# Optimization experiments

Hardware: AMD Instinct MI355X
Metric: run time of the kernel (lower is better)

## Reference

```python
import jax, jax.numpy as jnp
import numpy as np

B, S = 128, 64          # batch, sequence length (cities)
H = 128                 # hidden size
STATIC, DYNAMIC = 2, 2  # static/dynamic feature channels


def setup_inputs() -> dict:
    key = jax.random.key(0)
    ks = jax.random.split(key, 16)
    g = lambda k, shape: (jax.random.normal(k, shape, dtype=jnp.float32) * 0.1)
    return {
        "static": jax.random.normal(ks[0], (B, STATIC, S), dtype=jnp.float32),
        "dynamic": jax.random.uniform(ks[1], (B, DYNAMIC, S), dtype=jnp.float32),
        "x0": jnp.zeros((STATIC,), jnp.float32),           # learned initial decoder input
        "static_w": g(ks[2], (H, STATIC)),  "static_b": g(ks[3], (H,)),
        "dynamic_w": g(ks[4], (H, DYNAMIC)), "dynamic_b": g(ks[5], (H,)),
        "decoder_w": g(ks[6], (H, STATIC)), "decoder_b": g(ks[7], (H,)),
        "gru_wih": g(ks[8], (3 * H, H)), "gru_whh": g(ks[9], (3 * H, H)),
        "gru_bih": g(ks[10], (3 * H,)), "gru_bhh": g(ks[11], (3 * H,)),
        "attn_v": g(ks[12], (H,)), "attn_W": g(ks[13], (H, 3 * H)),
        "ptr_v": g(ks[14], (H,)),  "ptr_W": g(ks[15], (H, 2 * H)),
    }


def _forward(static, dynamic, x0, static_w, static_b, dynamic_w, dynamic_b,
             decoder_w, decoder_b, gru_wih, gru_whh, gru_bih, gru_bhh,
             attn_v, attn_W, ptr_v, ptr_W):
    Bsz, in_size, seq = static.shape
    # Conv1d with kernel_size=1 == pointwise channel mixing
    conv = lambda w, b, x: jnp.einsum('oi,bis->bos', w, x) + b[None, :, None]
    static_h = conv(static_w, static_b, static)      # [B,H,S]
    dynamic_h = conv(dynamic_w, dynamic_b, dynamic)  # [B,H,S]

    def gru_cell(x, h):
        # torch nn.GRU gate order: r, z, n
        gi = x @ gru_wih.T + gru_bih
        gh = h @ gru_whh.T + gru_bhh
        i_r, i_z, i_n = jnp.split(gi, 3, axis=1)
        h_r, h_z, h_n = jnp.split(gh, 3, axis=1)
        r = jax.nn.sigmoid(i_r + h_r)
        z = jax.nn.sigmoid(i_z + h_z)
        n = jnp.tanh(i_n + r * h_n)
        return (1.0 - z) * n + z * h

    def step(carry, _):
        dec_in, h = carry                                   # [B,in,1], [B,H]
        dec_h = conv(decoder_w, decoder_b, dec_in)[:, :, 0]  # [B,H]
        h_new = gru_cell(dec_h, h)                           # rnn_out == last_hh (1 layer)
        rnn_out = h_new
        # encoder attention over cities
        hid = jnp.concatenate(
            [static_h, dynamic_h,
             jnp.broadcast_to(rnn_out[:, :, None], static_h.shape)], axis=1)  # [B,3H,S]
        e = jnp.tanh(jnp.einsum('hk,bks->bhs', attn_W, hid))
        attns = jax.nn.softmax(jnp.einsum('h,bhs->bs', attn_v, e), axis=1)    # [B,S]
        context = jnp.einsum('bs,bhs->bh', attns, static_h)                   # [B,H]
        energy = jnp.concatenate(
            [static_h, jnp.broadcast_to(context[:, :, None], static_h.shape)], axis=1)
        logits = jnp.einsum('h,bhs->bs', ptr_v,
                            jnp.tanh(jnp.einsum('hk,bks->bhs', ptr_W, energy)))
        # mask_fn is None -> mask stays all ones -> mask.log() == 0
        logp_all = jax.nn.log_softmax(logits, axis=1)
        ptr = jnp.argmax(logp_all, axis=1)                  # greedy (eval mode)
        logp = jnp.take_along_axis(logp_all, ptr[:, None], axis=1)[:, 0]
        idx = jnp.broadcast_to(ptr[:, None, None], (Bsz, in_size, 1))
        new_in = jax.lax.stop_gradient(jnp.take_along_axis(static, idx, axis=2))
        return (new_in, h_new), (ptr, logp)

    dec0 = jnp.broadcast_to(x0[None, :, None], (Bsz, in_size, 1))
    h0 = jnp.zeros((Bsz, static_h.shape[1]), static.dtype)
    _, (ptrs, logps) = jax.lax.scan(step, (dec0, h0), None, length=seq)
    return ptrs.T, logps.T  # tour_idx [B,S] int, tour_logp [B,S] float


def reference(static, dynamic, x0, static_w, static_b, dynamic_w, dynamic_b,
              decoder_w, decoder_b, gru_wih, gru_whh, gru_bih, gru_bhh,
              attn_v, attn_W, ptr_v, ptr_W):
    return _forward(static, dynamic, x0, static_w, static_b, dynamic_w, dynamic_b,
                    decoder_w, decoder_b, gru_wih, gru_whh, gru_bih, gru_bhh,
                    attn_v, attn_W, ptr_v, ptr_W)
```

## Files before the change

### kernel.cpp

```cpp
#include <hip/hip_runtime.h>
#include <math.h>


#define K1  1.44269504088896340736f
#define K2  2.88539008177792681472f
#define LN2 0.69314718055994530942f

#define WS_M     0
#define WS_C     768
#define WS_PREA  1152
#define WS_PREP  (WS_PREA + 128*8192)
#define WS_Q     (WS_PREP + 128*8192)

template <int CTRL>
__device__ __forceinline__ float dppk(float x) {
  int xi = __builtin_bit_cast(int, x);
  return __builtin_bit_cast(float,
      __builtin_amdgcn_update_dpp(xi, xi, CTRL, 0xF, 0xF, false));
}
template <int CTRL>
__device__ __forceinline__ float dppz(float x) {
  int xi = __builtin_bit_cast(int, x);
  return __builtin_bit_cast(float,
      __builtin_amdgcn_update_dpp(0, xi, CTRL, 0xF, 0xF, true));
}
__device__ __forceinline__ float bcastf(float x, int lane) {
  return __builtin_bit_cast(float,
      __builtin_amdgcn_readlane(__builtin_bit_cast(int, x), lane));
}
__device__ __forceinline__ float sum4(float x) {
  x += dppk<0xB1>(x); x += dppk<0x4E>(x); return x;
}
__device__ __forceinline__ float sum8(float x) {
  x += dppk<0xB1>(x); x += dppk<0x4E>(x); x += dppk<0x141>(x); return x;
}
__device__ __forceinline__ float wsum64(float x) {
  x += dppz<0x111>(x); x += dppz<0x112>(x); x += dppz<0x114>(x);
  x += dppz<0x118>(x); x += dppz<0x142>(x); x += dppz<0x143>(x);
  return bcastf(x, 63);
}
__device__ __forceinline__ float wmax64(float x) {
  x = fmaxf(x, dppk<0x111>(x)); x = fmaxf(x, dppk<0x112>(x));
  x = fmaxf(x, dppk<0x114>(x)); x = fmaxf(x, dppk<0x118>(x));
  x = fmaxf(x, dppk<0x142>(x)); x = fmaxf(x, dppk<0x143>(x));
  return bcastf(x, 63);
}
#define RCP(x)  __builtin_amdgcn_rcpf(x)
#define EXP2(x) __builtin_amdgcn_exp2f(x)

__device__ __forceinline__ void bar_lds() {
  asm volatile("s_waitcnt lgkmcnt(0)" ::: "memory");
  __builtin_amdgcn_s_barrier();
  asm volatile("" ::: "memory");
}

__device__ __forceinline__ int rot8(int p) {
  return (p & 56) | ((p + (p >> 3)) & 7);
}

__global__ __launch_bounds__(256) void prep_small(
    const float* __restrict__ wih, const float* __restrict__ decw,
    const float* __restrict__ decb, const float* __restrict__ bih,
    float* __restrict__ ws) {
  int gid = blockIdx.x * 256 + threadIdx.x;
  if (gid < 384) {
    float m0 = 0.f, m1 = 0.f, cc = 0.f;
    for (int k = 0; k < 128; ++k) {
      float w = wih[gid * 128 + k];
      m0 += w * decw[k * 2 + 0];
      m1 += w * decw[k * 2 + 1];
      cc += w * decb[k];
    }
    ws[WS_M + gid * 2 + 0] = m0;
    ws[WS_M + gid * 2 + 1] = m1;
    ws[WS_C + gid] = cc + bih[gid];
  }
}

__global__ __launch_bounds__(256) void prep_big(
    const float* __restrict__ statics, const float* __restrict__ dynamics,
    const float* __restrict__ sw, const float* __restrict__ sb,
    const float* __restrict__ dw, const float* __restrict__ db,
    const float* __restrict__ attn_W, const float* __restrict__ ptr_W,
    float* __restrict__ ws) {
  __shared__ __align__(16) float sh[128 * 64];
  __shared__ __align__(16) float dh[128 * 64];
  __shared__ float st[128];
  __shared__ float dy[128];
  int b = blockIdx.x >> 3;
  int hq = blockIdx.x & 7;
  int t = threadIdx.x;
  if (t < 128) st[t] = statics[b * 128 + t];
  else         dy[t - 128] = dynamics[b * 128 + (t - 128)];
  __syncthreads();
  for (int e = t; e < 8192; e += 256) {
    int h = e >> 6, s = e & 63;
    sh[e] = sw[h * 2 + 0] * st[s] + sw[h * 2 + 1] * st[64 + s] + sb[h];
    dh[e] = dw[h * 2 + 0] * dy[s] + dw[h * 2 + 1] * dy[64 + s] + db[h];
  }
  __syncthreads();
  int hh = hq * 16 + (t >> 4);
  int s0 = (t & 15) * 4;
  float4 pA = {0, 0, 0, 0}, pP = {0, 0, 0, 0}, qq = {0, 0, 0, 0};
  for (int k = 0; k < 128; ++k) {
    float4 sv = *(const float4*)&sh[k * 64 + s0];
    float4 dv = *(const float4*)&dh[k * 64 + s0];
    float w1 = attn_W[hh * 384 + k];
    float w2 = attn_W[hh * 384 + 128 + k];
    float p1 = ptr_W[hh * 256 + k];
    float p2 = ptr_W[hh * 256 + 128 + k];
    pA.x += w1 * sv.x + w2 * dv.x;  pA.y += w1 * sv.y + w2 * dv.y;
    pA.z += w1 * sv.z + w2 * dv.z;  pA.w += w1 * sv.w + w2 * dv.w;
    pP.x += p1 * sv.x;  pP.y += p1 * sv.y;  pP.z += p1 * sv.z;  pP.w += p1 * sv.w;
    qq.x += p2 * sv.x;  qq.y += p2 * sv.y;  qq.z += p2 * sv.z;  qq.w += p2 * sv.w;
  }
  float4 eA, eP;
  eA.x = exp2f(K2 * pA.x); eA.y = exp2f(K2 * pA.y);
  eA.z = exp2f(K2 * pA.z); eA.w = exp2f(K2 * pA.w);
  eP.x = exp2f(K2 * pP.x); eP.y = exp2f(K2 * pP.y);
  eP.z = exp2f(K2 * pP.z); eP.w = exp2f(K2 * pP.w);
  int o = b * 8192 + hh * 64 + s0;
  *(float4*)&ws[WS_PREA + o] = eA;
  *(float4*)&ws[WS_PREP + o] = eP;
  *(float4*)&ws[WS_Q + o]    = qq;
}

__global__ __launch_bounds__(512)
__attribute__((amdgpu_waves_per_eu(2)))
void drl4tsp_main(
    const float* __restrict__ statics, const float* __restrict__ x0,
    const float* __restrict__ whh, const float* __restrict__ attn_W,
    const float* __restrict__ bhh_g, const float* __restrict__ attn_v,
    const float* __restrict__ ptr_v, const float* __restrict__ ws,
    float* __restrict__ out) {
  __shared__ float4 W3s4[128 * 32];
  __shared__ float4 EAT4[64 * 32];
  __shared__ float4 EPT4[64 * 32];
  __shared__ float4 uav3[64];
  __shared__ float4 uav2[64];
  __shared__ float4 gp4[128 * 3];
  __shared__ __align__(16) float hp[144];
  __shared__ __align__(16) float attns[64];
  __shared__ float a_lds[64];
  __shared__ float l_lds[64];
  __shared__ float stt[128];
  __shared__ float outbuf[64];
  __shared__ float Lhist[4096];

  const int b    = blockIdx.x;
  const int t    = threadIdx.x;
  const int lane = t & 63;
  const int g    = t >> 2;
  const int q    = t & 3;
  const int s    = t >> 3;
  const int hg   = t & 7;

  float wr0[32], wr1[32], wr2[32];
#pragma unroll
  for (int kk = 0; kk < 8; ++kk) {
    float4 a = *(const float4*)(whh + g * 128         + kk * 16 + q * 4);
    float4 c = *(const float4*)(whh + (128 + g) * 128 + kk * 16 + q * 4);
    float4 d = *(const float4*)(whh + (256 + g) * 128 + kk * 16 + q * 4);
    wr0[4*kk] = a.x; wr0[4*kk+1] = a.y; wr0[4*kk+2] = a.z; wr0[4*kk+3] = a.w;
    wr1[4*kk] = c.x; wr1[4*kk+1] = c.y; wr1[4*kk+2] = c.z; wr1[4*kk+3] = c.w;
    wr2[4*kk] = d.x; wr2[4*kk+1] = d.y; wr2[4*kk+2] = d.z; wr2[4*kk+3] = d.w;
  }
  float qr[16];
  {
    const float4* pq = (const float4*)(ws + WS_Q + b * 8192 + g * 64 + q * 16);
#pragma unroll
    for (int i = 0; i < 4; ++i) {
      float4 v = pq[i];
      qr[4*i] = v.x; qr[4*i+1] = v.y; qr[4*i+2] = v.z; qr[4*i+3] = v.w;
    }
  }

  {
    const float4* src = (const float4*)(attn_W + g * 384 + 256);
#pragma unroll
    for (int kk = 0; kk < 8; ++kk) {
      int j = q * 8 + kk;
      W3s4[g * 32 + ((j + 2 * g) & 31)] = src[j];
    }
  }
  for (int e = t; e < 8192; e += 512) {
    int h = e >> 6, sE = e & 63;
    int rg = ((h >> 2) + sE) & 31;
    ((float*)EAT4)[sE * 128 + rg * 4 + (h & 3)] = ws[WS_PREA + b * 8192 + e];
    ((float*)EPT4)[sE * 128 + rg * 4 + (h & 3)] = ws[WS_PREP + b * 8192 + e];
  }
  if (t < 128) {
    int h = t;
    int rg = rot8(h >> 1);
    ((float*)uav3)[rg * 4 + (h & 1) * 2 + 1] = 2.0f * attn_v[h];
    ((float*)uav2)[rg * 4 + (h & 1) * 2 + 1] = 2.0f * ptr_v[h];
    stt[h] = statics[b * 128 + h];
    const float* Mm = ws + WS_M;
    const float* Cc = ws + WS_C;
    float cR = Cc[h] + bhh_g[h];
    float cZ = Cc[128 + h] + bhh_g[128 + h];
    gp4[h*3 + 0] = float4{Mm[h*2], Mm[h*2+1], cR, Mm[(128+h)*2]};
    gp4[h*3 + 1] = float4{Mm[(128+h)*2+1], cZ, Mm[(256+h)*2], Mm[(256+h)*2+1]};
    gp4[h*3 + 2] = float4{Cc[256+h], bhh_g[256+h], 0.f, 0.f};
  }
  __syncthreads();

  float hreg = 0.f, ghr = 0.f, ghz = 0.f, ghn = 0.f;
  float d0 = x0[0], d1 = x0[1];

  for (int step = 0; step < 64; ++step) {
    {
      float4 v0 = gp4[g*3], v1 = gp4[g*3+1], v2 = gp4[g*3+2];
      float r = RCP(1.f + EXP2(-K1 * (v0.x*d0 + v0.y*d1 + v0.z + ghr)));
      float z = RCP(1.f + EXP2(-K1 * (v0.w*d0 + v1.x*d1 + v1.y + ghz)));
      float xn = v1.z*d0 + v1.w*d1 + v2.x + r * (ghn + v2.y);
      float n = 1.f - 2.f * RCP(EXP2(K2 * xn) + 1.f);
      hreg = (1.f - z) * n + z * hreg;
      if (q == 0) hp[(g >> 5) * 36 + (g & 31)] = hreg;
    }
    bar_lds();
    {
      float u3a = 0.f, u3b = 0.f;
#pragma unroll
      for (int kk = 0; kk < 8; ++kk) {
        float4 hv = *(const float4*)&hp[(kk >> 1) * 36 + (kk & 1) * 16 + q * 4];
        float4 wv = W3s4[g * 32 + ((kk * 4 + q + 2 * g) & 31)];
        float d2 = wv.x*hv.x + wv.y*hv.y + wv.z*hv.z + wv.w*hv.w;
        if (kk & 1) u3b += d2; else u3a += d2;
      }
      float u3 = sum4(u3a + u3b);
      if (q == 0)
        ((float*)uav3)[rot8(g >> 1) * 4 + (g & 1) * 2] = EXP2(K2 * u3);
    }
    bar_lds();
    float sr = 0.f, sz = 0.f, sn = 0.f;
    {
      float acc0 = 0.f, acc1 = 0.f;
#pragma unroll
      for (int ii = 0; ii < 4; ++ii) {
        float4 ea = EAT4[s * 32 + ((hg * 4 + ii + s) & 31)];
        int p0 = hg * 8 + 2 * ii;
        float4 ua = uav3[(p0 & 56) | ((p0 + hg) & 7)];
        float4 ub = uav3[((p0+1) & 56) | ((p0 + 1 + hg) & 7)];
        float x1 = ea.x * ua.x + 1.f, y1 = ea.y * ua.z + 1.f;
        acc0 += (ua.y * y1 + ua.w * x1) * RCP(x1 * y1);
        float x2 = ea.z * ub.x + 1.f, y2 = ea.w * ub.z + 1.f;
        acc1 += (ub.y * y2 + ub.w * x2) * RCP(x2 * y2);
      }
#pragma unroll
      for (int kk = 0; kk < 4; ++kk) {
        float4 hv = *(const float4*)&hp[(kk >> 1) * 36 + (kk & 1) * 16 + q * 4];
        int k = kk * 4;
        sr += wr0[k]*hv.x + wr0[k+1]*hv.y + wr0[k+2]*hv.z + wr0[k+3]*hv.w;
        sz += wr1[k]*hv.x + wr1[k+1]*hv.y + wr1[k+2]*hv.z + wr1[k+3]*hv.w;
        sn += wr2[k]*hv.x + wr2[k+1]*hv.y + wr2[k+2]*hv.z + wr2[k+3]*hv.w;
      }
      float acc = sum8(acc0 + acc1);
      if (hg == 0) a_lds[s] = -acc;
    }
    bar_lds();
    float4 ep0, ep1, ep2, ep3;
    {
      float a = a_lds[lane];
      ep0 = EPT4[s * 32 + ((hg * 4 + 0 + s) & 31)];
      ep1 = EPT4[s * 32 + ((hg * 4 + 1 + s) & 31)];
      ep2 = EPT4[s * 32 + ((hg * 4 + 2 + s) & 31)];
      ep3 = EPT4[s * 32 + ((hg * 4 + 3 + s) & 31)];
      float e = EXP2(K1 * a);
      attns[lane] = e;
#pragma unroll
      for (int kk = 4; kk < 8; ++kk) {
        float4 hv = *(const float4*)&hp[(kk >> 1) * 36 + (kk & 1) * 16 + q * 4];
        int k = kk * 4;
        sr += wr0[k]*hv.x + wr0[k+1]*hv.y + wr0[k+2]*hv.z + wr0[k+3]*hv.w;
        sz += wr1[k]*hv.x + wr1[k+1]*hv.y + wr1[k+2]*hv.z + wr1[k+3]*hv.w;
        sn += wr2[k]*hv.x + wr2[k+1]*hv.y + wr2[k+2]*hv.z + wr2[k+3]*hv.w;
      }
      float sum = wsum64(e);
      float p = 0.f;
#pragma unroll
      for (int ii = 0; ii < 4; ++ii) {
        float4 av = *(const float4*)&attns[q * 16 + ii * 4];
        p += qr[4*ii]*av.x + qr[4*ii+1]*av.y + qr[4*ii+2]*av.z + qr[4*ii+3]*av.w;
      }
      p *= RCP(sum);
      p = sum4(p);
      if (q == 0)
        ((float*)uav2)[rot8(g >> 1) * 4 + (g & 1) * 2] = EXP2(K2 * p);
      ghr = sum4(sr); ghz = sum4(sz); ghn = sum4(sn);
    }
    bar_lds();
    {
      float acc0 = 0.f, acc1 = 0.f;
#pragma unroll
      for (int ii = 0; ii < 4; ++ii) {
        float4 ep = (ii == 0) ? ep0 : (ii == 1) ? ep1 : (ii == 2) ? ep2 : ep3;
        int p0 = hg * 8 + 2 * ii;
        float4 ua = uav2[(p0 & 56) | ((p0 + hg) & 7)];
        float4 ub = uav2[((p0+1) & 56) | ((p0 + 1 + hg) & 7)];
        float x1 = ep.x * ua.x + 1.f, y1 = ep.y * ua.z + 1.f;
        acc0 += (ua.y * y1 + ua.w * x1) * RCP(x1 * y1);
        float x2 = ep.z * ub.x + 1.f, y2 = ep.w * ub.z + 1.f;
        acc1 += (ub.y * y2 + ub.w * x2) * RCP(x2 * y2);
      }
      float acc = sum8(acc0 + acc1);
      if (hg == 0) l_lds[s] = -acc;
    }
    bar_lds();
    {
      float L = l_lds[lane];
      float v = wmax64(L);
      unsigned long long mk = __ballot(L == v);
      int idx = __builtin_ctzll(mk);
      if (t < 64) Lhist[step * 64 + t] = L;
      if (t == 0) outbuf[step] = (float)idx;
      d0 = stt[idx];
      d1 = stt[64 + idx];
    }
  }
  bar_lds();
  {
    int wv = t >> 6;
    for (int st = wv; st < 64; st += 8) {
      float L = Lhist[st * 64 + lane];
      float v = wmax64(L);
      float e2 = EXP2(K1 * (L - v));
      float s3 = wsum64(e2);
      if (lane == 0)
        out[8192 + b * 64 + st] = -LN2 * __builtin_amdgcn_logf(s3);
      if (lane == 1)
        out[b * 64 + st] = outbuf[st];
    }
  }
}

extern "C" void kernel_launch(void* const* d_in, const int* in_sizes, int n_in,
                              void* d_out, int out_size, void* d_ws, size_t ws_size,
                              hipStream_t stream) {
  const float* statics  = (const float*)d_in[0];
  const float* dynamics = (const float*)d_in[1];
  const float* x0       = (const float*)d_in[2];
  const float* sw       = (const float*)d_in[3];
  const float* sb       = (const float*)d_in[4];
  const float* dw       = (const float*)d_in[5];
  const float* db       = (const float*)d_in[6];
  const float* decw     = (const float*)d_in[7];
  const float* decb     = (const float*)d_in[8];
  const float* wih      = (const float*)d_in[9];
  const float* whh      = (const float*)d_in[10];
  const float* bih      = (const float*)d_in[11];
  const float* bhh      = (const float*)d_in[12];
  const float* attn_v   = (const float*)d_in[13];
  const float* attn_W   = (const float*)d_in[14];
  const float* ptr_v    = (const float*)d_in[15];
  const float* ptr_W    = (const float*)d_in[16];
  float* ws  = (float*)d_ws;
  float* out = (float*)d_out;

  hipLaunchKernelGGL(prep_small, dim3(2), dim3(256), 0, stream,
                     wih, decw, decb, bih, ws);
  hipLaunchKernelGGL(prep_big, dim3(1024), dim3(256), 0, stream,
                     statics, dynamics, sw, sb, dw, db, attn_W, ptr_W, ws);
  hipLaunchKernelGGL(drl4tsp_main, dim3(128), dim3(512), 0, stream,
                     statics, x0, whh, attn_W, bhh, attn_v, ptr_v, ws, out);
}
```

Baseline: 194.0 us.

## Remap attention/pointer energy reduction to 16 lanes x 2 cities per thread

Reorganizes the per-step attention and pointer energy sums so each thread covers two sequence positions over a quarter of the hidden dimension, with 16-lane groups instead of 8. The swizzled LDS layout of the precomputed energy tiles is changed to match, so each uav vector is loaded once and reused for two cities, cutting LDS reads per thread. The cost is a longer 16-lane DPP reduction that now runs for two accumulators, plus float2 stores of the results.

```diff
diff --git a/kernel.cpp b/kernel.cpp
--- a/kernel.cpp
+++ b/kernel.cpp
@@ -31,8 +31,9 @@
 __device__ __forceinline__ float sum4(float x) {
   x += dppk<0xB1>(x); x += dppk<0x4E>(x); return x;
 }
-__device__ __forceinline__ float sum8(float x) {
-  x += dppk<0xB1>(x); x += dppk<0x4E>(x); x += dppk<0x141>(x); return x;
+__device__ __forceinline__ float sum16(float x) {
+  x += dppk<0xB1>(x); x += dppk<0x4E>(x); x += dppk<0x141>(x); x += dppk<0x128>(x);
+  return x;
 }
 __device__ __forceinline__ float wsum64(float x) {
   x += dppz<0x111>(x); x += dppz<0x112>(x); x += dppz<0x114>(x);
@@ -141,8 +142,8 @@
   __shared__ float4 gp4[128 * 3];
   __shared__ __align__(16) float hp[144];
   __shared__ __align__(16) float attns[64];
-  __shared__ float a_lds[64];
-  __shared__ float l_lds[64];
+  __shared__ __align__(16) float a_lds[64];
+  __shared__ __align__(16) float l_lds[64];
   __shared__ float stt[128];
   __shared__ float outbuf[64];
   __shared__ float Lhist[4096];
@@ -152,8 +153,10 @@
   const int lane = t & 63;
   const int g    = t >> 2;
   const int q    = t & 3;
-  const int s    = t >> 3;
-  const int hg   = t & 7;
+  const int hgx  = lane & 15;
+  const int sq   = lane >> 4;
+  const int s0   = (t >> 6) * 8 + sq * 2;
+  const int posb = (hgx + ((sq & 1) << 4)) & 31;
 
   float wr0[32], wr1[32], wr2[32];
 #pragma unroll
@@ -185,9 +188,11 @@
   }
   for (int e = t; e < 8192; e += 512) {
     int h = e >> 6, sE = e & 63;
-    int rg = ((h >> 2) + sE) & 31;
-    ((float*)EAT4)[sE * 128 + rg * 4 + (h & 3)] = ws[WS_PREA + b * 8192 + e];
-    ((float*)EPT4)[sE * 128 + rg * 4 + (h & 3)] = ws[WS_PREP + b * 8192 + e];
+    int gi = h >> 2;
+    int pos = ((gi >> 1) + ((gi & 1) << 4) + (((sE >> 1) & 1) << 4)) & 31;
+    int idx = sE * 128 + pos * 4 + (h & 3);
+    ((float*)EAT4)[idx] = ws[WS_PREA + b * 8192 + e];
+    ((float*)EPT4)[idx] = ws[WS_PREP + b * 8192 + e];
   }
   if (t < 128) {
     int h = t;
@@ -237,15 +242,19 @@
     {
       float acc0 = 0.f, acc1 = 0.f;
 #pragma unroll
-      for (int ii = 0; ii < 4; ++ii) {
-        float4 ea = EAT4[s * 32 + ((hg * 4 + ii + s) & 31)];
-        int p0 = hg * 8 + 2 * ii;
-        float4 ua = uav3[(p0 & 56) | ((p0 + hg) & 7)];
-        float4 ub = uav3[((p0+1) & 56) | ((p0 + 1 + hg) & 7)];
-        float x1 = ea.x * ua.x + 1.f, y1 = ea.y * ua.z + 1.f;
-        acc0 += (ua.y * y1 + ua.w * x1) * RCP(x1 * y1);
-        float x2 = ea.z * ub.x + 1.f, y2 = ea.w * ub.z + 1.f;
-        acc1 += (ub.y * y2 + ub.w * x2) * RCP(x2 * y2);
+      for (int j = 0; j < 2; ++j) {
+        float4 uvA = uav3[rot8(hgx * 4 + 2 * j)];
+        float4 uvB = uav3[rot8(hgx * 4 + 2 * j + 1)];
+        int pos = (posb + 16 * j) & 31;
+#pragma unroll
+        for (int ss = 0; ss < 2; ++ss) {
+          float4 ea = EAT4[(s0 + ss) * 32 + pos];
+          float x1 = ea.x * uvA.x + 1.f, y1 = ea.y * uvA.z + 1.f;
+          float x2 = ea.z * uvB.x + 1.f, y2 = ea.w * uvB.z + 1.f;
+          float r1 = (uvA.y * y1 + uvA.w * x1) * RCP(x1 * y1);
+          float r2 = (uvB.y * y2 + uvB.w * x2) * RCP(x2 * y2);
+          if (ss == 0) acc0 += r1 + r2; else acc1 += r1 + r2;
+        }
       }
 #pragma unroll
       for (int kk = 0; kk < 4; ++kk) {
@@ -255,17 +264,18 @@
         sz += wr1[k]*hv.x + wr1[k+1]*hv.y + wr1[k+2]*hv.z + wr1[k+3]*hv.w;
         sn += wr2[k]*hv.x + wr2[k+1]*hv.y + wr2[k+2]*hv.z + wr2[k+3]*hv.w;
       }
-      float acc = sum8(acc0 + acc1);
-      if (hg == 0) a_lds[s] = -acc;
+      acc0 = sum16(acc0);
+      acc1 = sum16(acc1);
+      if (hgx == 0) *(float2*)&a_lds[s0] = float2{-acc0, -acc1};
     }
     bar_lds();
     float4 ep0, ep1, ep2, ep3;
     {
       float a = a_lds[lane];
-      ep0 = EPT4[s * 32 + ((hg * 4 + 0 + s) & 31)];
-      ep1 = EPT4[s * 32 + ((hg * 4 + 1 + s) & 31)];
-      ep2 = EPT4[s * 32 + ((hg * 4 + 2 + s) & 31)];
-      ep3 = EPT4[s * 32 + ((hg * 4 + 3 + s) & 31)];
+      ep0 = EPT4[(s0 + 0) * 32 + posb];
+      ep1 = EPT4[(s0 + 1) * 32 + posb];
+      ep2 = EPT4[(s0 + 0) * 32 + ((posb + 16) & 31)];
+      ep3 = EPT4[(s0 + 1) * 32 + ((posb + 16) & 31)];
       float e = EXP2(K1 * a);
       attns[lane] = e;
 #pragma unroll
@@ -293,18 +303,23 @@
     {
       float acc0 = 0.f, acc1 = 0.f;
 #pragma unroll
-      for (int ii = 0; ii < 4; ++ii) {
-        float4 ep = (ii == 0) ? ep0 : (ii == 1) ? ep1 : (ii == 2) ? ep2 : ep3;
-        int p0 = hg * 8 + 2 * ii;
-        float4 ua = uav2[(p0 & 56) | ((p0 + hg) & 7)];
-        float4 ub = uav2[((p0+1) & 56) | ((p0 + 1 + hg) & 7)];
-        float x1 = ep.x * ua.x + 1.f, y1 = ep.y * ua.z + 1.f;
-        acc0 += (ua.y * y1 + ua.w * x1) * RCP(x1 * y1);
-        float x2 = ep.z * ub.x + 1.f, y2 = ep.w * ub.z + 1.f;
-        acc1 += (ub.y * y2 + ub.w * x2) * RCP(x2 * y2);
-      }
-      float acc = sum8(acc0 + acc1);
-      if (hg == 0) l_lds[s] = -acc;
+      for (int j = 0; j < 2; ++j) {
+        float4 uvA = uav2[rot8(hgx * 4 + 2 * j)];
+        float4 uvB = uav2[rot8(hgx * 4 + 2 * j + 1)];
+#pragma unroll
+        for (int ss = 0; ss < 2; ++ss) {
+          float4 ep = (j == 0) ? (ss == 0 ? ep0 : ep1)
+                               : (ss == 0 ? ep2 : ep3);
+          float x1 = ep.x * uvA.x + 1.f, y1 = ep.y * uvA.z + 1.f;
+          float x2 = ep.z * uvB.x + 1.f, y2 = ep.w * uvB.z + 1.f;
+          float r1 = (uvA.y * y1 + uvA.w * x1) * RCP(x1 * y1);
+          float r2 = (uvB.y * y2 + uvB.w * x2) * RCP(x2 * y2);
+          if (ss == 0) acc0 += r1 + r2; else acc1 += r1 + r2;
+        }
+      }
+      acc0 = sum16(acc0);
+      acc1 = sum16(acc1);
+      if (hgx == 0) *(float2*)&l_lds[s0] = float2{-acc0, -acc1};
     }
     bar_lds();
     {
```

Result: slower. 197.9 us (+2.0%).
